# Performance work log

Measured on AMD Instinct MI355X. Metric: run time of the kernel, lower is better.

Reference implementation:

```python
import jax, jax.numpy as jnp
import numpy as np

B, INSIZE, H, OUT, STEPS = 8192, 256, 128, 1, 50


def setup_inputs() -> dict:
    key = jax.random.key(0)
    ks = jax.random.split(key, 16)
    s = 0.05
    inp = {
        "x": jax.random.normal(ks[0], (B, INSIZE), jnp.float32),
        # encoder MLP: 256 -> 128 -> 128 -> 128 (ReLU on hiddens, linear out)
        "ew0": jax.random.normal(ks[1], (INSIZE, 128), jnp.float32) * s,
        "eb0": jnp.zeros((128,), jnp.float32),
        "ew1": jax.random.normal(ks[2], (128, 128), jnp.float32) * s,
        "eb1": jnp.zeros((128,), jnp.float32),
        "ew2": jax.random.normal(ks[3], (128, H), jnp.float32) * s,
        "eb2": jnp.zeros((H,), jnp.float32),
        # GRU (input size OUT=1, hidden H=128), PyTorch layout [3H, in]/[3H, H]
        "w_ih": jax.random.normal(ks[4], (3 * H, OUT), jnp.float32) * s,
        "w_hh": jax.random.normal(ks[5], (3 * H, H), jnp.float32) * s,
        "b_ih": jnp.zeros((3 * H,), jnp.float32),
        "b_hh": jnp.zeros((3 * H,), jnp.float32),
        # decoder MLP: 128 -> 16 -> 1
        "dw0": jax.random.normal(ks[6], (H, 16), jnp.float32) * s,
        "db0": jnp.zeros((16,), jnp.float32),
        "dw1": jax.random.normal(ks[7], (16, OUT), jnp.float32) * s,
        "db1": jnp.zeros((OUT,), jnp.float32),
    }
    return inp


def _gru_cell(x_t, h, w_ih, w_hh, b_ih, b_hh):
    # PyTorch GRU cell: gates ordered [r, z, n]
    gx = x_t @ w_ih.T + b_ih  # [B, 3H]
    gh = h @ w_hh.T + b_hh    # [B, 3H]
    r = jax.nn.sigmoid(gx[:, :H] + gh[:, :H])
    z = jax.nn.sigmoid(gx[:, H:2 * H] + gh[:, H:2 * H])
    n = jnp.tanh(gx[:, 2 * H:] + r * gh[:, 2 * H:])
    return (1.0 - z) * n + z * h


def reference(x, ew0, eb0, ew1, eb1, ew2, eb2, w_ih, w_hh, b_ih, b_hh, dw0, db0, dw1, db1):
    # encoder MLP -> initial hidden state
    h = jax.nn.relu(x @ ew0 + eb0)
    h = jax.nn.relu(h @ ew1 + eb1)
    h = h @ ew2 + eb2  # [B, H]

    def step(carry, _):
        prev, hc = carry
        hn = _gru_cell(prev, hc, w_ih, w_hh, b_ih, b_hh)
        d = jax.nn.relu(hn @ dw0 + db0)
        out = d @ dw1 + db1  # [B, 1]
        return (out, hn), out

    prev0 = jnp.zeros((x.shape[0], OUT), x.dtype)
    _, outs = jax.lax.scan(step, (prev0, h), None, length=STEPS)  # [50, B, 1]
    outs = jnp.squeeze(outs, -1).T  # [B, 50]
    # torch: cat([zeros, out_0..out_49], dim=1)[..., :-1] -> [zeros, out_0..out_48]
    zeros = jnp.zeros((x.shape[0], 1), x.dtype)
    return jnp.concatenate([zeros, outs], axis=1)[:, :-1]
```

## Files before the change

### kernel.cpp

```cpp
#include <hip/hip_runtime.h>

#define NTH 256

typedef _Float16 half8 __attribute__((ext_vector_type(8)));
typedef _Float16 half4 __attribute__((ext_vector_type(4)));
typedef __attribute__((ext_vector_type(4))) float floatx4;

#define LOG2E 1.44269504088896340736f

template<int CTRL>
__device__ __forceinline__ float dpp_add(float v) {
    int o = __builtin_amdgcn_update_dpp(0, __float_as_int(v), CTRL, 0xF, 0xF, true);
    return v + __int_as_float(o);
}

#define MFMA16 __builtin_amdgcn_mfma_f32_16x16x32_f16

template<int KTILES, int CMASK, int ROWH>
__device__ __forceinline__ void enc_layer(const _Float16* __restrict__ src,
                                          const float* __restrict__ W,
                                          const float* __restrict__ bias,
                                          int w, int quad, int l15,
                                          floatx4 acc[2]) {
    half8 bw[2][KTILES];
    #pragma unroll
    for (int nt = 0; nt < 2; nt++) {
        const int jc = w * 32 + nt * 16 + l15;
        #pragma unroll
        for (int kt = 0; kt < KTILES; kt++) {
            const int kb = kt * 32 + quad * 8;
            half8 hv;
            #pragma unroll
            for (int e = 0; e < 8; e++) hv[e] = (_Float16)W[(kb + e) * 128 + jc];
            bw[nt][kt] = hv;
        }
        const float bv = bias[jc];
        acc[nt] = (floatx4){bv, bv, bv, bv};
    }
    #pragma unroll
    for (int kt = 0; kt < KTILES; kt++) {
        const half8 av = *(const half8*)(src + l15 * ROWH +
                                         (((kt * 4 + quad) + l15) & CMASK) * 8);
        acc[0] = MFMA16(av, bw[0][kt], acc[0], 0, 0, 0);
        acc[1] = MFMA16(av, bw[1][kt], acc[1], 0, 0, 0);
    }
}

__device__ __forceinline__ void enc_store(_Float16* __restrict__ dst,
                                          const floatx4 acc[2],
                                          int w, int quad, int l15, bool relu) {
    #pragma unroll
    for (int nt = 0; nt < 2; nt++) {
        const int jc = w * 32 + nt * 16 + l15;
        #pragma unroll
        for (int reg = 0; reg < 4; reg++) {
            const int row = quad * 4 + reg;
            float v = acc[nt][reg];
            if (relu) v = fmaxf(v, 0.f);
            dst[row * 128 + ((((jc >> 3) + row) & 15) << 3) + (jc & 7)] = (_Float16)v;
        }
    }
}

__global__ __launch_bounds__(NTH, 2)
void gru_fused_kernel(const float* __restrict__ x,
                      const float* __restrict__ ew0, const float* __restrict__ eb0,
                      const float* __restrict__ ew1, const float* __restrict__ eb1,
                      const float* __restrict__ ew2, const float* __restrict__ eb2,
                      const float* __restrict__ w_ih, const float* __restrict__ w_hh,
                      const float* __restrict__ b_ih, const float* __restrict__ b_hh,
                      const float* __restrict__ dw0, const float* __restrict__ db0,
                      const float* __restrict__ dw1, const float* __restrict__ db1,
                      float* __restrict__ out) {
    __shared__ __align__(16) _Float16 encx[16 * 256];
    __shared__ __align__(16) _Float16 h1b[16 * 128];
    __shared__ __align__(16) _Float16 h16[2 * 16 * 128];
    __shared__ float outb[16][52];

    const int tid  = threadIdx.x;
    const int b0   = blockIdx.x * 16;
    const int lane = tid & 63;
    const int w    = tid >> 6;
    const int quad = lane >> 4;
    const int l15  = lane & 15;

    #pragma unroll
    for (int i = 0; i < 4; i++) {
        const int e = tid + i * NTH;
        const int row = e >> 6, c4 = e & 63;
        const float4 xv = *(const float4*)(x + (size_t)(b0 + row) * 256 + c4 * 4);
        half4 hv = {(_Float16)xv.x, (_Float16)xv.y, (_Float16)xv.z, (_Float16)xv.w};
        *(half4*)(encx + row * 256 + (((c4 >> 1) + row) & 31) * 8 + (c4 & 1) * 4) = hv;
    }
    __syncthreads();

    floatx4 ea[2];
    enc_layer<8, 31, 256>(encx, ew0, eb0, w, quad, l15, ea);
    enc_store(h1b, ea, w, quad, l15, true);
    __syncthreads();
    enc_layer<4, 15, 128>(h1b, ew1, eb1, w, quad, l15, ea);
    enc_store(encx, ea, w, quad, l15, true);
    __syncthreads();
    enc_layer<4, 15, 128>(encx, ew2, eb2, w, quad, l15, ea);
    float hold[2][4];
    #pragma unroll
    for (int nt = 0; nt < 2; nt++)
        #pragma unroll
        for (int reg = 0; reg < 4; reg++) hold[nt][reg] = ea[nt][reg];
    enc_store(h16, ea, w, quad, l15, false);
    if (tid < 16) outb[tid][0] = 0.f;

    half8 wb16[3][2][4];
    #pragma unroll
    for (int g = 0; g < 3; g++) {
        const float scale = (g == 2) ? 2.f * LOG2E : LOG2E;
        #pragma unroll
        for (int nt = 0; nt < 2; nt++) {
            const float* wrow = w_hh + (g * 128 + w * 32 + nt * 16 + l15) * 128;
            #pragma unroll
            for (int kt = 0; kt < 4; kt++) {
                const int kb = kt * 32 + quad * 8;
                half8 hv;
                #pragma unroll
                for (int e = 0; e < 8; e++) hv[e] = (_Float16)(wrow[kb + e] * scale);
                wb16[g][nt][kt] = hv;
            }
        }
    }
    half8 dw16[4];
    #pragma unroll
    for (int kt = 0; kt < 4; kt++) {
        half8 hv;
        #pragma unroll
        for (int e = 0; e < 8; e++)
            hv[e] = (_Float16)dw0[(kt * 32 + quad * 8 + e) * 16 + l15];
        dw16[kt] = hv;
    }
    float wr[2], wz[2], wn[2], c_r[2], c_z[2], c_n[2], bnih[2];
    int jcw[2];
    #pragma unroll
    for (int nt = 0; nt < 2; nt++) {
        const int jc = w * 32 + nt * 16 + l15;
        jcw[nt]  = jc;
        wr[nt]   = w_ih[jc] * LOG2E;
        wz[nt]   = w_ih[128 + jc] * LOG2E;
        wn[nt]   = w_ih[256 + jc] * (2.f * LOG2E);
        c_r[nt]  = (b_ih[jc] + b_hh[jc]) * LOG2E;
        c_z[nt]  = (b_ih[128 + jc] + b_hh[128 + jc]) * LOG2E;
        c_n[nt]  = b_hh[256 + jc] * (2.f * LOG2E);
        bnih[nt] = b_ih[256 + jc] * (2.f * LOG2E);
    }
    const float db0r = db0[l15];
    const float dw1r = dw1[l15];
    const float db1r = db1[0];
    __syncthreads();

    for (int t = 0; t <= 49; t++) {
        const int cur = t & 1, nxt = cur ^ 1;
        const _Float16* __restrict__ hc = h16 + cur * 2048;
        _Float16* __restrict__ hw = h16 + nxt * 2048;

        half8 ah[4];
        #pragma unroll
        for (int kt = 0; kt < 4; kt++)
            ah[kt] = *(const half8*)(hc + l15 * 128 +
                                     (((kt * 4 + quad) + l15) & 15) * 8);

        floatx4 dacc = (floatx4){0.f, 0.f, 0.f, 0.f};
        #pragma unroll
        for (int kt = 0; kt < 4; kt++)
            dacc = MFMA16(ah[kt], dw16[kt], dacc, 0, 0, 0);

        floatx4 acc[3][2];
        #pragma unroll
        for (int nt = 0; nt < 2; nt++) {
            acc[0][nt] = (floatx4){c_r[nt], c_r[nt], c_r[nt], c_r[nt]};
            acc[1][nt] = (floatx4){c_z[nt], c_z[nt], c_z[nt], c_z[nt]};
            acc[2][nt] = (floatx4){c_n[nt], c_n[nt], c_n[nt], c_n[nt]};
        }
        #pragma unroll
        for (int kt = 0; kt < 4; kt++)
            #pragma unroll
            for (int g = 0; g < 3; g++) {
                acc[g][0] = MFMA16(ah[kt], wb16[g][0][kt], acc[g][0], 0, 0, 0);
                acc[g][1] = MFMA16(ah[kt], wb16[g][1][kt], acc[g][1], 0, 0, 0);
            }

        float xp[4];
        #pragma unroll
        for (int reg = 0; reg < 4; reg++) {
            float v = fmaxf(dacc[reg] + db0r, 0.f) * dw1r;
            v = dpp_add<0x140>(v);
            v = dpp_add<0x141>(v);
            v = dpp_add<0x4E>(v);
            v = dpp_add<0xB1>(v);
            xp[reg] = (t == 0) ? 0.f : (v + db1r);
        }
        if (t > 0 && w == 0 && l15 == 0) {
            #pragma unroll
            for (int reg = 0; reg < 4; reg++)
                outb[quad * 4 + reg][t] = xp[reg];
        }

        if (t < 49) {
            #pragma unroll
            for (int nt = 0; nt < 2; nt++)
                #pragma unroll
                for (int reg = 0; reg < 4; reg++) {
                    const int row = quad * 4 + reg;
                    const float xpv = xp[reg];
                    const float hv0 = hold[nt][reg];
                    float gr = fmaf(xpv, wr[nt], acc[0][nt][reg]);
                    float gz = fmaf(xpv, wz[nt], acc[1][nt][reg]);
                    float Er = __builtin_amdgcn_exp2f(-gr);
                    float rg = __builtin_amdgcn_rcpf(1.f + Er);
                    float ys = fmaf(rg, acc[2][nt][reg], fmaf(xpv, wn[nt], bnih[nt]));
                    float Ey = __builtin_amdgcn_exp2f(ys);
                    float Ez = __builtin_amdgcn_exp2f(-gz);
                    float num = fmaf(Ez, Ey, -Ez) + fmaf(hv0, Ey, hv0);
                    float den = fmaf(Ey, Ez, Ey) + (Ez + 1.f);
                    const float hn = num * __builtin_amdgcn_rcpf(den);
                    hold[nt][reg] = hn;
                    hw[row * 128 + ((((jcw[nt] >> 3) + row) & 15) << 3) +
                       (jcw[nt] & 7)] = (_Float16)hn;
                }
        }
        __syncthreads();
    }

    for (int e = tid; e < 16 * 50; e += NTH) {
        const int b = e / 50;
        const int tcol = e - b * 50;
        out[(size_t)b0 * 50 + e] = outb[b][tcol];
    }
}

extern "C" void kernel_launch(void* const* d_in, const int* in_sizes, int n_in,
                              void* d_out, int out_size, void* d_ws, size_t ws_size,
                              hipStream_t stream) {
    const float* x   = (const float*)d_in[0];
    const float* ew0 = (const float*)d_in[1];
    const float* eb0 = (const float*)d_in[2];
    const float* ew1 = (const float*)d_in[3];
    const float* eb1 = (const float*)d_in[4];
    const float* ew2 = (const float*)d_in[5];
    const float* eb2 = (const float*)d_in[6];
    const float* wih = (const float*)d_in[7];
    const float* whh = (const float*)d_in[8];
    const float* bih = (const float*)d_in[9];
    const float* bhh = (const float*)d_in[10];
    const float* dw0 = (const float*)d_in[11];
    const float* db0 = (const float*)d_in[12];
    const float* dw1 = (const float*)d_in[13];
    const float* db1 = (const float*)d_in[14];
    float* out = (float*)d_out;

    gru_fused_kernel<<<512, NTH, 0, stream>>>(
        x, ew0, eb0, ew1, eb1, ew2, eb2, wih, whh, bih, bhh,
        dw0, db0, dw1, db1, out);
}
```

Baseline: 160.5 us.

## Precompute LDS offsets, split decoder MFMA chain, vectorize weight loads, raise priority

Loads the recurrent weights with float4 vector loads during setup. Moves the LDS read and write address calculations out of the 50-step loop into per-thread registers. Splits the decoder MFMA accumulation into two independent chains, with the bias folded into the initial accumulator, so the dependent MFMA chain is shorter. Simplifies the GRU output algebra to fewer operations and raises wave priority around the elementwise gate section. These changes add register pressure for the precomputed offsets in exchange for fewer ALU instructions on the serial per-step path.

```diff
diff --git a/kernel.cpp b/kernel.cpp
--- a/kernel.cpp
+++ b/kernel.cpp
@@ -120,9 +120,13 @@
             #pragma unroll
             for (int kt = 0; kt < 4; kt++) {
                 const int kb = kt * 32 + quad * 8;
+                const float4 w0 = *(const float4*)(wrow + kb);
+                const float4 w1 = *(const float4*)(wrow + kb + 4);
                 half8 hv;
-                #pragma unroll
-                for (int e = 0; e < 8; e++) hv[e] = (_Float16)(wrow[kb + e] * scale);
+                hv[0] = (_Float16)(w0.x * scale); hv[1] = (_Float16)(w0.y * scale);
+                hv[2] = (_Float16)(w0.z * scale); hv[3] = (_Float16)(w0.w * scale);
+                hv[4] = (_Float16)(w1.x * scale); hv[5] = (_Float16)(w1.y * scale);
+                hv[6] = (_Float16)(w1.z * scale); hv[7] = (_Float16)(w1.w * scale);
                 wb16[g][nt][kt] = hv;
             }
         }
@@ -137,11 +141,9 @@
         dw16[kt] = hv;
     }
     float wr[2], wz[2], wn[2], c_r[2], c_z[2], c_n[2], bnih[2];
-    int jcw[2];
-    #pragma unroll
-    for (int nt = 0; nt < 2; nt++) {
-        const int jc = w * 32 + nt * 16 + l15;
-        jcw[nt]  = jc;
+    #pragma unroll
+    for (int nt = 0; nt < 2; nt++) {
+        const int jc = w * 32 + nt * 16 + l15;
         wr[nt]   = w_ih[jc] * LOG2E;
         wz[nt]   = w_ih[128 + jc] * LOG2E;
         wn[nt]   = w_ih[256 + jc] * (2.f * LOG2E);
@@ -153,6 +155,21 @@
     const float db0r = db0[l15];
     const float dw1r = dw1[l15];
     const float db1r = db1[0];
+
+    int rdo[4];
+    #pragma unroll
+    for (int kt = 0; kt < 4; kt++)
+        rdo[kt] = l15 * 128 + (((kt * 4 + quad) + l15) & 15) * 8;
+    int wro[2][4];
+    #pragma unroll
+    for (int nt = 0; nt < 2; nt++) {
+        const int jc = w * 32 + nt * 16 + l15;
+        #pragma unroll
+        for (int reg = 0; reg < 4; reg++) {
+            const int row = quad * 4 + reg;
+            wro[nt][reg] = row * 128 + ((((jc >> 3) + row) & 15) << 3) + (jc & 7);
+        }
+    }
     __syncthreads();
 
     for (int t = 0; t <= 49; t++) {
@@ -163,13 +180,14 @@
         half8 ah[4];
         #pragma unroll
         for (int kt = 0; kt < 4; kt++)
-            ah[kt] = *(const half8*)(hc + l15 * 128 +
-                                     (((kt * 4 + quad) + l15) & 15) * 8);
-
-        floatx4 dacc = (floatx4){0.f, 0.f, 0.f, 0.f};
-        #pragma unroll
-        for (int kt = 0; kt < 4; kt++)
-            dacc = MFMA16(ah[kt], dw16[kt], dacc, 0, 0, 0);
+            ah[kt] = *(const half8*)(hc + rdo[kt]);
+
+        floatx4 dacc0 = (floatx4){db0r, db0r, db0r, db0r};
+        floatx4 dacc1 = (floatx4){0.f, 0.f, 0.f, 0.f};
+        dacc0 = MFMA16(ah[0], dw16[0], dacc0, 0, 0, 0);
+        dacc1 = MFMA16(ah[1], dw16[1], dacc1, 0, 0, 0);
+        dacc0 = MFMA16(ah[2], dw16[2], dacc0, 0, 0, 0);
+        dacc1 = MFMA16(ah[3], dw16[3], dacc1, 0, 0, 0);
 
         floatx4 acc[3][2];
         #pragma unroll
@@ -186,10 +204,12 @@
                 acc[g][1] = MFMA16(ah[kt], wb16[g][1][kt], acc[g][1], 0, 0, 0);
             }
 
+        __builtin_amdgcn_s_setprio(1);
+
         float xp[4];
         #pragma unroll
         for (int reg = 0; reg < 4; reg++) {
-            float v = fmaxf(dacc[reg] + db0r, 0.f) * dw1r;
+            float v = fmaxf(dacc0[reg] + dacc1[reg], 0.f) * dw1r;
             v = dpp_add<0x140>(v);
             v = dpp_add<0x141>(v);
             v = dpp_add<0x4E>(v);
@@ -207,24 +227,25 @@
             for (int nt = 0; nt < 2; nt++)
                 #pragma unroll
                 for (int reg = 0; reg < 4; reg++) {
-                    const int row = quad * 4 + reg;
                     const float xpv = xp[reg];
                     const float hv0 = hold[nt][reg];
                     float gr = fmaf(xpv, wr[nt], acc[0][nt][reg]);
                     float gz = fmaf(xpv, wz[nt], acc[1][nt][reg]);
                     float Er = __builtin_amdgcn_exp2f(-gr);
+                    float Ez = __builtin_amdgcn_exp2f(-gz);
                     float rg = __builtin_amdgcn_rcpf(1.f + Er);
                     float ys = fmaf(rg, acc[2][nt][reg], fmaf(xpv, wn[nt], bnih[nt]));
                     float Ey = __builtin_amdgcn_exp2f(ys);
-                    float Ez = __builtin_amdgcn_exp2f(-gz);
-                    float num = fmaf(Ez, Ey, -Ez) + fmaf(hv0, Ey, hv0);
-                    float den = fmaf(Ey, Ez, Ey) + (Ez + 1.f);
+                    float u   = Ey + 1.f;
+                    float t1  = fmaf(Ez, Ey, -Ez);
+                    float num = fmaf(hv0, u, t1);
+                    float den = fmaf(Ez, u, u);
                     const float hn = num * __builtin_amdgcn_rcpf(den);
                     hold[nt][reg] = hn;
-                    hw[row * 128 + ((((jcw[nt] >> 3) + row) & 15) << 3) +
-                       (jcw[nt] & 7)] = (_Float16)hn;
+                    hw[wro[nt][reg]] = (_Float16)hn;
                 }
         }
+        __builtin_amdgcn_s_setprio(0);
         __syncthreads();
     }
 
```

After: 157.9 us. About the same (-1.6%).
